# Performance work log

Hardware: AMD Instinct MI355X
Metric: run time of the kernel (lower is better)

## Reference

```python
import jax, jax.numpy as jnp
import numpy as np

FACTOR = 5


def setup_inputs() -> dict:
    key = jax.random.key(0)
    k1, k2, k3, k4 = jax.random.split(key, 4)
    B, L, H, D = 2, 4096, 8, 64
    sample_k = min(FACTOR * int(np.ceil(np.log(L))), L)  # 45
    return {
        "queries": jax.random.normal(k1, (B, L, H, D), dtype=jnp.float32),
        "keys": jax.random.normal(k2, (B, L, H, D), dtype=jnp.float32),
        "values": jax.random.normal(k3, (B, L, H, D), dtype=jnp.float32),
        "attn_mask": jnp.zeros((1,), dtype=bool),  # unused; ProbMask is built internally
        "index_sample": jax.random.randint(k4, (L, sample_k), 0, L, dtype=jnp.int32),
    }


def reference(queries, keys, values, attn_mask, index_sample):
    # queries/keys/values: [B, L, H, D] -> [B, H, L, D]
    Q = jnp.swapaxes(queries, 1, 2)
    K = jnp.swapaxes(keys, 1, 2)
    V = jnp.swapaxes(values, 1, 2)
    B, H, L_Q, D = Q.shape
    L_K = K.shape[2]
    n_top = min(FACTOR * int(np.ceil(np.log(L_Q))), L_Q)
    scale = 1.0 / jnp.sqrt(jnp.float32(D))

    # --- sparse measurement: sampled QK scores ---
    # K_sample[b,h,q,s,d] = K[b,h,index_sample[q,s],d]
    K_sample = K[:, :, index_sample, :]                       # [B,H,L_Q,S,D]
    QK_sample = jnp.einsum("bhqd,bhqsd->bhqs", Q, K_sample)   # [B,H,L_Q,S]
    M = QK_sample.max(axis=-1) - QK_sample.sum(axis=-1) / L_K  # sparsity measure

    # --- top-u query selection ---
    _, M_top = jax.lax.top_k(M, n_top)                         # [B,H,u]
    Q_reduce = jnp.take_along_axis(Q, M_top[..., None], axis=2)  # [B,H,u,D]

    # --- full scores for selected queries ---
    scores = jnp.einsum("bhud,bhkd->bhuk", Q_reduce, K) * scale  # [B,H,u,L_K]

    # mask_flag=True: causal ProbMask (key pos > selected query pos)
    key_pos = jnp.arange(L_K)
    causal = key_pos[None, None, None, :] > M_top[..., None]
    scores = jnp.where(causal, -jnp.inf, scores)
    attn = jax.nn.softmax(scores, axis=-1)

    # --- initial context (cumsum, masked case) + scatter update ---
    context = jnp.cumsum(V, axis=2)                            # [B,H,L_Q,D]
    ctx_sel = jnp.einsum("bhuk,bhkd->bhud", attn, V)
    b_idx = jnp.arange(B)[:, None, None]
    h_idx = jnp.arange(H)[None, :, None]
    context = context.at[b_idx, h_idx, M_top].set(ctx_sel)
    return jnp.swapaxes(context, 1, 2)  # [B, L_Q, H, D]
```

## Files before the change

### kernel.cpp

```cpp
#include <hip/hip_runtime.h>
#include <math.h>

#define B_    2
#define L_    4096
#define H_    8
#define D_    64
#define S_    45
#define NT_   45
#define BH_   16
#define CHV   64
#define NCHV  64
#define KC    128
#define SCALE 0.125f
#define NEG_BIG (-1e30f)

#define OFF_M     0
#define OFF_MTOP  65536
#define OFF_T     66304
#define OFF_CTX   67072
#define OFF_VSUM  131072
#define NZERO     46848

typedef __attribute__((ext_vector_type(8))) short s8b;
typedef __attribute__((ext_vector_type(4))) float f32x4;

template <int CTRL>
__device__ __forceinline__ float dpp_ror_f(float x) {
    int y = __builtin_amdgcn_update_dpp(0, __float_as_int(x), CTRL, 0xF, 0xF, false);
    return __int_as_float(y);
}

__device__ __forceinline__ unsigned f2bf(float x) {
    return (__float_as_uint(x) >> 16);
}
__device__ __forceinline__ float bflo(unsigned u) { return __uint_as_float(u << 16); }
__device__ __forceinline__ float bfhi(unsigned u) { return __uint_as_float(u & 0xffff0000u); }

__global__ __launch_bounds__(256) void k1(const float* __restrict__ Q,
                                          const float* __restrict__ Kt,
                                          const float* __restrict__ V,
                                          const int* __restrict__ samp,
                                          float* __restrict__ ws)
{
    int tid  = threadIdx.x;
    int w    = tid >> 6;
    int lane = tid & 63;

    if (blockIdx.x < 4096) {
        int i   = blockIdx.x;
        int xcd = i & 7;
        int b   = xcd >> 2;
        int hh  = (xcd >> 1) & 1;
        int qq  = ((i >> 3) << 1) | (xcd & 1);

        __shared__ int soff[4][S_];
        if (tid < 4 * S_) {
            int qs = tid / S_, ss = tid - qs * S_;
            soff[qs][ss] = (samp[(qq * 4 + qs) * S_ + ss] << 11) | (hh << 10);
        }
        __syncthreads();

        int q  = qq * 4 + w;
        int h4 = lane >> 4;

        const float4 q4 = *(const float4*)(Q +
            ((((long)b * L_ + q) * H_ + hh * 4) << 6) + lane * 4);

        const char* kslab = (const char*)Kt + (long)b * (L_ * 2048);
        unsigned lb = (unsigned)(lane * 16);

        float mx = NEG_BIG, sm = 0.f;
#pragma unroll
        for (int jb = 0; jb < 45; jb += 15) {
            float4 kb[15];
#pragma unroll
            for (int j = 0; j < 15; ++j)
                kb[j] = *(const float4*)(kslab +
                        ((unsigned)soff[w][jb + j] + lb));
#pragma unroll
            for (int j = 0; j < 15; ++j) {
                float p = q4.x * kb[j].x + q4.y * kb[j].y +
                          q4.z * kb[j].z + q4.w * kb[j].w;
                p += dpp_ror_f<0x121>(p);
                p += dpp_ror_f<0x122>(p);
                p += dpp_ror_f<0x124>(p);
                p += dpp_ror_f<0x128>(p);
                mx = fmaxf(mx, p);
                sm += p;
            }
        }
        if ((lane & 15) == 0)
            ws[OFF_M + ((long)(b * 8 + hh * 4 + h4)) * L_ + q] =
                mx - sm * (1.0f / (float)L_);
    } else {
        int unit = (blockIdx.x - 4096) * 4 + w;
        int bh = unit >> 6, ch = unit & 63;
        int b = bh >> 3, h = bh & 7;
        const float* vp = V + ((((long)b * L_ + (long)ch * CHV) * H_ + h) << 6) + lane;
        float ssum = 0.f;
#pragma unroll
        for (int ib = 0; ib < CHV; ib += 16) {
            float vb[16];
#pragma unroll
            for (int j = 0; j < 16; ++j) vb[j] = vp[(long)(ib + j) * (H_ * D_)];
#pragma unroll
            for (int j = 0; j < 16; ++j) ssum += vb[j];
        }
        ws[OFF_VSUM + unit * 64 + lane] = ssum;
    }
}

__global__ __launch_bounds__(256) void k2(float* __restrict__ ws)
{
    int tid  = threadIdx.x;
    int w    = tid >> 6;
    int lane = tid & 63;

    for (int i = blockIdx.x * 256 + tid; i < NZERO; i += 16 * 256)
        ws[OFF_T + i] = 0.f;

    int bh = blockIdx.x;
    int* Mtop = (int*)ws + OFF_MTOP + bh * NT_;

    __shared__ float lv_[4][NT_];
    __shared__ int   li_[4][NT_];

    const float4* m4 = (const float4*)(ws + OFF_M + (long)bh * L_ +
                                       w * 1024 + lane * 16);
    float vals[16];
    {
        float4 a = m4[0], bq = m4[1], c = m4[2], d = m4[3];
        vals[0]=a.x; vals[1]=a.y; vals[2]=a.z; vals[3]=a.w;
        vals[4]=bq.x; vals[5]=bq.y; vals[6]=bq.z; vals[7]=bq.w;
        vals[8]=c.x; vals[9]=c.y; vals[10]=c.z; vals[11]=c.w;
        vals[12]=d.x; vals[13]=d.y; vals[14]=d.z; vals[15]=d.w;
    }
    float lv = NEG_BIG; int li = lane * 16;
#pragma unroll
    for (int j = 0; j < 16; ++j)
        if (vals[j] > lv) { lv = vals[j]; li = lane * 16 + j; }

    for (int r = 0; r < NT_; ++r) {
        float rm = lv;
        rm = fmaxf(rm, dpp_ror_f<0x121>(rm));
        rm = fmaxf(rm, dpp_ror_f<0x122>(rm));
        rm = fmaxf(rm, dpp_ror_f<0x124>(rm));
        rm = fmaxf(rm, dpp_ror_f<0x128>(rm));
        rm = fmaxf(rm, __shfl_xor(rm, 16));
        rm = fmaxf(rm, __shfl_xor(rm, 32));
        unsigned long long bm = __ballot(lv == rm);
        int winner = __ffsll(bm) - 1;
        int wi = __shfl(li, winner);
        if (lane == 0) { lv_[w][r] = rm; li_[w][r] = w * 1024 + wi; }
        if (lane == winner) {
#pragma unroll
            for (int j = 0; j < 16; ++j)
                if (j == (wi & 15)) vals[j] = NEG_BIG;
            lv = NEG_BIG; li = lane * 16;
#pragma unroll
            for (int j = 0; j < 16; ++j)
                if (vals[j] > lv) { lv = vals[j]; li = lane * 16 + j; }
        }
    }
    __syncthreads();

    if (w == 0) {
        int g = lane & 3;
        int p = 0;
        float hv = lv_[g][0]; int hi = li_[g][0];
        for (int r = 0; r < NT_; ++r) {
            float v0 = __shfl(hv, 0), v1 = __shfl(hv, 1),
                  v2 = __shfl(hv, 2), v3 = __shfl(hv, 3);
            int   i0 = __shfl(hi, 0), i1 = __shfl(hi, 1),
                  i2 = __shfl(hi, 2), i3 = __shfl(hi, 3);
            float bv = v0; int bi = i0, bg = 0;
            if (v1 > bv) { bv = v1; bi = i1; bg = 1; }
            if (v2 > bv) { bv = v2; bi = i2; bg = 2; }
            if (v3 > bv) { bv = v3; bi = i3; bg = 3; }
            if (lane == 0) Mtop[r] = bi;
            if (g == bg) {
                ++p;
                hv = (p < NT_) ? lv_[g][p] : NEG_BIG;
                hi = (p < NT_) ? li_[g][p] : 0;
            }
        }
    }
}

#define KPAD16 72
#define PSTR   136
__global__ __launch_bounds__(256) void k3(const float* __restrict__ Q,
                                          const float* __restrict__ Kt,
                                          const float* __restrict__ V,
                                          float* __restrict__ out,
                                          float* __restrict__ ws)
{
    __shared__ unsigned short Klds16[KC * KPAD16];
    __shared__ unsigned short Qs16[32 * KPAD16];
    __shared__ unsigned short P16[32 * PSTR];
    __shared__ int qposs[32];

    int tid = threadIdx.x;

    if (blockIdx.x < 1024) {
        int bh = blockIdx.x >> 6;
        int kc = (blockIdx.x >> 1) & 31;
        int ug = blockIdx.x & 1;
        int b = bh >> 3, h = bh & 7;
        int kbase = kc * KC;
        int u0 = ug * 23;
        int NU = ug ? 22 : 23;

        if (tid < 32) {
            int uu = tid < NU ? tid : NU - 1;
            qposs[tid] = ((const int*)ws)[OFF_MTOP + bh * NT_ + tid < NU ? OFF_MTOP + bh * NT_ + u0 + uu : OFF_MTOP + bh * NT_ + u0 + uu];
        }
        if (tid < 32) {
            int uu = tid < NU ? tid : NU - 1;
            qposs[tid] = ((const int*)ws)[OFF_MTOP + bh * NT_ + u0 + uu];
        }
        __syncthreads();

        {
            const float4* ksrc4 = (const float4*)(Kt + ((((long)b * L_ + kbase) * H_ + h) << 6));
#pragma unroll
            for (int i = 0; i < 8; ++i) {
                int e = i * 256 + tid;
                int r = e >> 4, c4 = e & 15;
                float4 kv = ksrc4[(long)r * (H_ * D_ / 4) + c4];
                uint2 pk;
                pk.x = (__float_as_uint(kv.x) >> 16) | (__float_as_uint(kv.y) & 0xffff0000u);
                pk.y = (__float_as_uint(kv.z) >> 16) | (__float_as_uint(kv.w) & 0xffff0000u);
                *(uint2*)&Klds16[r * KPAD16 + ((c4 * 4) ^ ((r & 7) << 3))] = pk;
            }
#pragma unroll
            for (int i = 0; i < 2; ++i) {
                int e = i * 256 + tid;
                int r = e >> 4, c4 = e & 15;
                int qp = qposs[r];
                const float4* qsrc4 = (const float4*)(Q + ((((long)b * L_ + qp) * H_ + h) << 6));
                float4 qv = qsrc4[c4];
                uint2 pk;
                pk.x = (__float_as_uint(qv.x) >> 16) | (__float_as_uint(qv.y) & 0xffff0000u);
                pk.y = (__float_as_uint(qv.z) >> 16) | (__float_as_uint(qv.w) & 0xffff0000u);
                *(uint2*)&Qs16[r * KPAD16 + ((c4 * 4) ^ ((r & 7) << 3))] = pk;
            }
        }
        __syncthreads();

        {
            int lane = tid & 63, w = tid >> 6;
            int c = lane & 15, hi = lane >> 4;
            int t = w & 1, Hh = w >> 1;
            int slot = t * 16 + c;
            int qp = qposs[slot];

            s8b bq0 = *(const s8b*)&Qs16[slot * KPAD16 + ((hi * 8) ^ ((slot & 7) << 3))];
            s8b bq1 = *(const s8b*)&Qs16[slot * KPAD16 + ((32 + hi * 8) ^ ((slot & 7) << 3))];

            f32x4 acc0 = {0.f,0.f,0.f,0.f}, acc1 = acc0, acc2 = acc0, acc3 = acc0;
#define QK_TILE(MT, ACC)                                                      \
            {                                                                 \
                int kr = Hh * 64 + (MT) * 16 + c;                             \
                s8b a0 = *(const s8b*)&Klds16[kr * KPAD16 +                   \
                            ((hi * 8) ^ ((kr & 7) << 3))];                    \
                s8b a1 = *(const s8b*)&Klds16[kr * KPAD16 +                   \
                            ((32 + hi * 8) ^ ((kr & 7) << 3))];               \
                ACC = __builtin_amdgcn_mfma_f32_16x16x32_bf16(a0, bq0, ACC, 0, 0, 0); \
                ACC = __builtin_amdgcn_mfma_f32_16x16x32_bf16(a1, bq1, ACC, 0, 0, 0); \
            }
            QK_TILE(0, acc0)
            QK_TILE(1, acc1)
            QK_TILE(2, acc2)
            QK_TILE(3, acc3)
#undef QK_TILE

            float ssum = 0.f;
#pragma unroll
            for (int mt = 0; mt < 4; ++mt) {
                f32x4 a = mt == 0 ? acc0 : (mt == 1 ? acc1 : (mt == 2 ? acc2 : acc3));
                float e[4];
#pragma unroll
                for (int reg = 0; reg < 4; ++reg) {
                    int kpos = kbase + Hh * 64 + mt * 16 + hi * 4 + reg;
                    e[reg] = (kpos > qp) ? 0.f : __expf(a[reg] * SCALE);
                    ssum += e[reg];
                }
                uint2 pk;
                pk.x = f2bf(e[0]) | (f2bf(e[1]) << 16);
                pk.y = f2bf(e[2]) | (f2bf(e[3]) << 16);
                *(uint2*)&P16[slot * PSTR + Hh * 64 + mt * 16 + hi * 4] = pk;
            }
            ssum += __shfl_xor(ssum, 16);
            ssum += __shfl_xor(ssum, 32);
            if (hi == 0) {
                int sl = t * 16 + c;
                if (sl < NU)
                    atomicAdd(&ws[OFF_T + bh * NT_ + u0 + sl], ssum);
            }
        }
        __syncthreads();

        {
            int lane = tid & 63, w = tid >> 6;
            const float* vsrc = V + ((((long)b * L_ + kbase) * H_ + h) << 6);
            float ctx[6];
#pragma unroll
            for (int j = 0; j < 6; ++j) ctx[j] = 0.f;
            for (int kk8 = 0; kk8 < 16; ++kk8) {
                float v[8];
#pragma unroll
                for (int t = 0; t < 8; ++t)
                    v[t] = vsrc[(long)(kk8 * 8 + t) * (H_ * D_) + lane];
#pragma unroll
                for (int j = 0; j < 6; ++j) {
                    int ul = w + j * 4;
                    if (ul < NU) {
                        uint4 U = *(const uint4*)&P16[ul * PSTR + kk8 * 8];
                        ctx[j] += bflo(U.x) * v[0] + bfhi(U.x) * v[1]
                                + bflo(U.y) * v[2] + bfhi(U.y) * v[3]
                                + bflo(U.z) * v[4] + bfhi(U.z) * v[5]
                                + bflo(U.w) * v[6] + bfhi(U.w) * v[7];
                    }
                }
            }
#pragma unroll
            for (int j = 0; j < 6; ++j) {
                int ul = w + j * 4;
                if (ul < NU)
                    atomicAdd(&ws[OFF_CTX + ((long)(bh * NT_ + u0 + ul) << 6) + lane], ctx[j]);
            }
        }
    } else {
        int w    = tid >> 6;
        int lane = tid & 63;
        int unit = (blockIdx.x - 1024) * 4 + w;
        int bh = unit >> 6, ch = unit & 63;
        int b = bh >> 3, h = bh & 7;
        int d = lane;

        float acc = 0.f;
        {
            const float* vs = ws + OFF_VSUM + (long)bh * NCHV * 64 + d;
            int c = 0;
            for (; c + 8 <= ch; c += 8) {
                float vb[8];
#pragma unroll
                for (int j = 0; j < 8; ++j) vb[j] = vs[(c + j) * 64];
#pragma unroll
                for (int j = 0; j < 8; ++j) acc += vb[j];
            }
            for (; c < ch; ++c) acc += vs[c * 64];
        }

        const float* vp = V   + ((((long)b * L_ + (long)ch * CHV) * H_ + h) << 6) + d;
        float*       op = out + ((((long)b * L_ + (long)ch * CHV) * H_ + h) << 6) + d;
#pragma unroll
        for (int ib = 0; ib < CHV; ib += 16) {
            float vb[16];
#pragma unroll
            for (int j = 0; j < 16; ++j) vb[j] = vp[(long)(ib + j) * (H_ * D_)];
#pragma unroll
            for (int j = 0; j < 16; ++j) {
                acc += vb[j];
                op[(long)(ib + j) * (H_ * D_)] = acc;
            }
        }
    }
}

__global__ __launch_bounds__(256) void kD(float* __restrict__ out,
                                          const float* __restrict__ ws)
{
    int tid  = threadIdx.x;
    int w    = tid >> 6;
    int lane = tid & 63;
    int unit = blockIdx.x * 4 + w;
    int bh = unit / NT_;
    int b = bh >> 3, h = bh & 7;

    float T   = ws[OFF_T + unit];
    float ctx = ws[OFF_CTX + ((long)unit << 6) + lane];
    int   qp  = ((const int*)ws)[OFF_MTOP + unit];
    out[((((long)b * L_ + qp) * H_ + h) << 6) + lane] = ctx / T;
}

extern "C" void kernel_launch(void* const* d_in, const int* in_sizes, int n_in,
                              void* d_out, int out_size, void* d_ws, size_t ws_size,
                              hipStream_t stream)
{
    const float* Q    = (const float*)d_in[0];
    const float* K    = (const float*)d_in[1];
    const float* V    = (const float*)d_in[2];
    const int*   samp = (const int*)d_in[4];
    float* out = (float*)d_out;
    float* ws  = (float*)d_ws;

    k1<<<4352, 256, 0, stream>>>(Q, K, V, samp, ws);
    k2<<<16, 256, 0, stream>>>(ws);
    k3<<<1280, 256, 0, stream>>>(Q, K, V, out, ws);
    kD<<<180, 256, 0, stream>>>(out, ws);
}
```

Measured before the change: 182.0 us.

## Replace iterative argmax top-k with radix threshold search in single wave

The top-k selection kernel previously ran 45 rounds of wave-wide argmax reductions across four waves, then merged the results in shared memory. It now uses one wave per (b,h). That wave converts the scores to order-preserving unsigned keys and binary-searches the 45th-largest threshold with 32 counting passes, then uses a prefix scan to compact the indices. This removes the serial 45-round loop and the cross-wave merge, at the cost of 64 keys held in registers per lane. The output is no longer sorted by score, but downstream code only uses the set of selected indices. A duplicated load of the selected query positions in k3 is also dropped.

Result: faster. 170.0 us (-6.6%).

```diff
diff --git a/kernel.cpp b/kernel.cpp
--- a/kernel.cpp
+++ b/kernel.cpp
@@ -29,6 +29,10 @@
     int y = __builtin_amdgcn_update_dpp(0, __float_as_int(x), CTRL, 0xF, 0xF, false);
     return __int_as_float(y);
 }
+template <int CTRL>
+__device__ __forceinline__ int dpp_ror_i(int x) {
+    return __builtin_amdgcn_update_dpp(0, x, CTRL, 0xF, 0xF, false);
+}
 
 __device__ __forceinline__ unsigned f2bf(float x) {
     return (__float_as_uint(x) >> 16);
@@ -113,76 +117,70 @@
 __global__ __launch_bounds__(256) void k2(float* __restrict__ ws)
 {
     int tid  = threadIdx.x;
-    int w    = tid >> 6;
     int lane = tid & 63;
 
     for (int i = blockIdx.x * 256 + tid; i < NZERO; i += 16 * 256)
         ws[OFF_T + i] = 0.f;
+    if (tid >= 64) return;
 
     int bh = blockIdx.x;
+
+    const uint4* m4 = (const uint4*)(ws + OFF_M + (long)bh * L_ + lane * 64);
+    unsigned key[64];
+#pragma unroll
+    for (int j4 = 0; j4 < 16; ++j4) {
+        uint4 kv = m4[j4];
+        unsigned uu[4] = {kv.x, kv.y, kv.z, kv.w};
+#pragma unroll
+        for (int e = 0; e < 4; ++e) {
+            unsigned u = uu[e];
+            key[j4 * 4 + e] = (u & 0x80000000u) ? ~u : (u | 0x80000000u);
+        }
+    }
+
+    unsigned lo = 0u, hi = 0xFFFFFFFFu;
+    for (int it = 0; it < 32; ++it) {
+        unsigned d = hi - lo;
+        unsigned mid = lo + (d >> 1) + (d & 1);
+        int cnt = 0;
+#pragma unroll
+        for (int j = 0; j < 64; ++j) cnt += (key[j] >= mid) ? 1 : 0;
+        cnt += dpp_ror_i<0x121>(cnt);
+        cnt += dpp_ror_i<0x122>(cnt);
+        cnt += dpp_ror_i<0x124>(cnt);
+        cnt += dpp_ror_i<0x128>(cnt);
+        cnt += __shfl_xor(cnt, 16);
+        cnt += __shfl_xor(cnt, 32);
+        if (cnt >= NT_) lo = mid; else hi = mid - 1;
+    }
+    unsigned lam = lo;
+
+    int cgt = 0, ceq = 0;
+#pragma unroll
+    for (int j = 0; j < 64; ++j) {
+        cgt += (key[j] > lam) ? 1 : 0;
+        ceq += (key[j] == lam) ? 1 : 0;
+    }
+    int packed = (cgt << 16) | ceq;
+    int incl = packed;
+#pragma unroll
+    for (int off = 1; off < 64; off <<= 1) {
+        int t = __shfl_up(incl, off);
+        if (lane >= off) incl += t;
+    }
+    int excl = incl - packed;
+    int ngt_total = __shfl(incl, 63) >> 16;
+
     int* Mtop = (int*)ws + OFF_MTOP + bh * NT_;
-
-    __shared__ float lv_[4][NT_];
-    __shared__ int   li_[4][NT_];
-
-    const float4* m4 = (const float4*)(ws + OFF_M + (long)bh * L_ +
-                                       w * 1024 + lane * 16);
-    float vals[16];
-    {
-        float4 a = m4[0], bq = m4[1], c = m4[2], d = m4[3];
-        vals[0]=a.x; vals[1]=a.y; vals[2]=a.z; vals[3]=a.w;
-        vals[4]=bq.x; vals[5]=bq.y; vals[6]=bq.z; vals[7]=bq.w;
-        vals[8]=c.x; vals[9]=c.y; vals[10]=c.z; vals[11]=c.w;
-        vals[12]=d.x; vals[13]=d.y; vals[14]=d.z; vals[15]=d.w;
-    }
-    float lv = NEG_BIG; int li = lane * 16;
-#pragma unroll
-    for (int j = 0; j < 16; ++j)
-        if (vals[j] > lv) { lv = vals[j]; li = lane * 16 + j; }
-
-    for (int r = 0; r < NT_; ++r) {
-        float rm = lv;
-        rm = fmaxf(rm, dpp_ror_f<0x121>(rm));
-        rm = fmaxf(rm, dpp_ror_f<0x122>(rm));
-        rm = fmaxf(rm, dpp_ror_f<0x124>(rm));
-        rm = fmaxf(rm, dpp_ror_f<0x128>(rm));
-        rm = fmaxf(rm, __shfl_xor(rm, 16));
-        rm = fmaxf(rm, __shfl_xor(rm, 32));
-        unsigned long long bm = __ballot(lv == rm);
-        int winner = __ffsll(bm) - 1;
-        int wi = __shfl(li, winner);
-        if (lane == 0) { lv_[w][r] = rm; li_[w][r] = w * 1024 + wi; }
-        if (lane == winner) {
-#pragma unroll
-            for (int j = 0; j < 16; ++j)
-                if (j == (wi & 15)) vals[j] = NEG_BIG;
-            lv = NEG_BIG; li = lane * 16;
-#pragma unroll
-            for (int j = 0; j < 16; ++j)
-                if (vals[j] > lv) { lv = vals[j]; li = lane * 16 + j; }
-        }
-    }
-    __syncthreads();
-
-    if (w == 0) {
-        int g = lane & 3;
-        int p = 0;
-        float hv = lv_[g][0]; int hi = li_[g][0];
-        for (int r = 0; r < NT_; ++r) {
-            float v0 = __shfl(hv, 0), v1 = __shfl(hv, 1),
-                  v2 = __shfl(hv, 2), v3 = __shfl(hv, 3);
-            int   i0 = __shfl(hi, 0), i1 = __shfl(hi, 1),
-                  i2 = __shfl(hi, 2), i3 = __shfl(hi, 3);
-            float bv = v0; int bi = i0, bg = 0;
-            if (v1 > bv) { bv = v1; bi = i1; bg = 1; }
-            if (v2 > bv) { bv = v2; bi = i2; bg = 2; }
-            if (v3 > bv) { bv = v3; bi = i3; bg = 3; }
-            if (lane == 0) Mtop[r] = bi;
-            if (g == bg) {
-                ++p;
-                hv = (p < NT_) ? lv_[g][p] : NEG_BIG;
-                hi = (p < NT_) ? li_[g][p] : 0;
-            }
+    int gpos = excl >> 16;
+    int epos = ngt_total + (excl & 0xFFFF);
+#pragma unroll
+    for (int j = 0; j < 64; ++j) {
+        if (key[j] > lam) {
+            Mtop[gpos++] = lane * 64 + j;
+        } else if (key[j] == lam) {
+            if (epos < NT_) Mtop[epos] = lane * 64 + j;
+            ++epos;
         }
     }
 }
@@ -211,10 +209,6 @@
         int u0 = ug * 23;
         int NU = ug ? 22 : 23;
 
-        if (tid < 32) {
-            int uu = tid < NU ? tid : NU - 1;
-            qposs[tid] = ((const int*)ws)[OFF_MTOP + bh * NT_ + tid < NU ? OFF_MTOP + bh * NT_ + u0 + uu : OFF_MTOP + bh * NT_ + u0 + uu];
-        }
         if (tid < 32) {
             int uu = tid < NU ? tid : NU - 1;
             qposs[tid] = ((const int*)ws)[OFF_MTOP + bh * NT_ + u0 + uu];
```
